# Optimization experiments

Hardware: AMD Instinct MI355X
Metric: run time of the kernel (lower is better)

The kernel has to match this reference:

```python
import jax, jax.numpy as jnp
import numpy as np

NUM_HEADS = 12
H = W = 64            # spatial grid (SAM ViT-B global attention)
DIM = 768
HEAD_DIM = DIM // NUM_HEADS


def setup_inputs() -> dict:
    key = jax.random.key(0)
    ks = jax.random.split(key, 7)
    return {
        "x": jax.random.normal(ks[0], (1, H, W, DIM), dtype=jnp.float32),
        "qkv_w": jax.random.normal(ks[1], (3 * DIM, DIM), dtype=jnp.float32) * 0.02,
        "qkv_b": jax.random.normal(ks[2], (3 * DIM,), dtype=jnp.float32) * 0.02,
        "proj_w": jax.random.normal(ks[3], (DIM, DIM), dtype=jnp.float32) * 0.02,
        "proj_b": jax.random.normal(ks[4], (DIM,), dtype=jnp.float32) * 0.02,
        "rel_pos_h": jax.random.normal(ks[5], (2 * H - 1, HEAD_DIM), dtype=jnp.float32) * 0.02,
        "rel_pos_w": jax.random.normal(ks[6], (2 * W - 1, HEAD_DIM), dtype=jnp.float32) * 0.02,
    }


def _get_rel_pos(size: int, rel_pos: jnp.ndarray) -> jnp.ndarray:
    # q_size == k_size == size; rel_pos already has length 2*size-1 (no interp).
    coords = jnp.arange(size)[:, None] - jnp.arange(size)[None, :] + (size - 1)
    return rel_pos[coords]  # [size, size, head_dim]


def reference(x, qkv_w, qkv_b, proj_w, proj_b, rel_pos_h, rel_pos_w):
    B, h, w, C = x.shape
    nh, hd = NUM_HEADS, C // NUM_HEADS
    S = h * w
    scale = hd ** -0.5

    qkv = x.reshape(B, S, C) @ qkv_w.T + qkv_b            # [B, S, 3C]
    qkv = qkv.reshape(B, S, 3, nh, hd).transpose(2, 0, 3, 1, 4)
    qkv = qkv.reshape(3, B * nh, S, hd)
    q, k, v = qkv[0], qkv[1], qkv[2]                      # [B*nh, S, hd]

    attn = jnp.einsum('bqc,bkc->bqk', q * scale, k)       # [B*nh, S, S]

    Rh = _get_rel_pos(h, rel_pos_h)                       # [h, h, hd]
    Rw = _get_rel_pos(w, rel_pos_w)                       # [w, w, hd]
    r_q = q.reshape(B * nh, h, w, hd)
    rel_h = jnp.einsum('bhwc,hkc->bhwk', r_q, Rh)         # [B*nh, h, w, h]
    rel_w = jnp.einsum('bhwc,wkc->bhwk', r_q, Rw)         # [B*nh, h, w, w]
    attn = (attn.reshape(B * nh, h, w, h, w)
            + rel_h[:, :, :, :, None]
            + rel_w[:, :, :, None, :]).reshape(B * nh, S, S)

    attn = jax.nn.softmax(attn, axis=-1)
    out = jnp.einsum('bqk,bkc->bqc', attn, v)             # [B*nh, S, hd]
    out = out.reshape(B, nh, h, w, hd).transpose(0, 2, 3, 1, 4).reshape(B, h, w, C)
    return out @ proj_w.T + proj_b
```

## Files before the change

### kernel.cpp

```cpp
#include <hip/hip_runtime.h>


typedef __bf16 bf16;
typedef __bf16 bf16x8 __attribute__((ext_vector_type(8)));
typedef __bf16 bf16x4 __attribute__((ext_vector_type(4)));
typedef float f32x4 __attribute__((ext_vector_type(4)));
typedef float f32x16 __attribute__((ext_vector_type(16)));
typedef unsigned int u32;

__device__ __forceinline__ f32x4 mfma16(bf16x8 a, bf16x8 b, f32x4 c) {
  return __builtin_amdgcn_mfma_f32_16x16x32_bf16(a, b, c, 0, 0, 0);
}
__device__ __forceinline__ f32x16 mfma32(bf16x8 a, bf16x8 b, f32x16 c) {
  return __builtin_amdgcn_mfma_f32_32x32x16_bf16(a, b, c, 0, 0, 0);
}

typedef const __attribute__((address_space(1))) void* gas_ptr;
typedef __attribute__((address_space(3))) void* las_ptr;
__device__ __forceinline__ void gl_lds16(const void* g, void* l) {
  __builtin_amdgcn_global_load_lds((gas_ptr)g, (las_ptr)l, 16, 0, 0);
}

#define L2E 1.4426950408889634f

__global__ __launch_bounds__(256) void cvt3(
    const float* __restrict__ a, bf16* __restrict__ oa,
    const float* __restrict__ b, bf16* __restrict__ ob,
    const float* __restrict__ c, bf16* __restrict__ oc) {
  int blk = blockIdx.x;
  const float* src;
  bf16* dst;
  int base;
  if (blk < 1536)       { src = a; dst = oa; base = blk; }
  else if (blk < 2400)  { src = b; dst = ob; base = blk - 1536; }
  else                  { src = c; dst = oc; base = blk - 2400; }
  int idx = (base * 256 + threadIdx.x) * 8;
  f32x4 x = *(const f32x4*)&src[idx];
  f32x4 y = *(const f32x4*)&src[idx + 4];
  bf16x8 o;
#pragma unroll
  for (int j = 0; j < 4; j++) { o[j] = (bf16)x[j]; o[j + 4] = (bf16)y[j]; }
  *(bf16x8*)&dst[idx] = o;
}

template <int MODE>
__global__ __launch_bounds__(256) void gemm128(
    const bf16* __restrict__ A, const bf16* __restrict__ B,
    const float* __restrict__ bias, int K, int N,
    bf16* __restrict__ q_s, bf16* __restrict__ k_s, bf16* __restrict__ v_t,
    float* __restrict__ outf) {
  __shared__ __align__(16) bf16 lbuf[2][128 * 32];
  bf16* lA = lbuf[0];
  bf16* lB = lbuf[1];
  const int tid = threadIdx.x;
  const int w = tid >> 6, l = tid & 63;
  const int n0 = blockIdx.x * 128, m0 = blockIdx.y * 128;

  f32x4 acc[4][4] = {};

  const int ch0 = w * 2, ch1 = ch0 + 1;
  const int r0 = ch0 * 16 + (l >> 2), r1 = ch1 * 16 + (l >> 2);
  const int ce = (l & 3) * 8;
  const int mw = (w & 1) * 64, nw = (w >> 1) * 64;

  for (int k0 = 0; k0 < K; k0 += 32) {
    __syncthreads();
    gl_lds16(&A[(size_t)(m0 + r0) * K + k0 + ce], &lA[ch0 * 512]);
    gl_lds16(&A[(size_t)(m0 + r1) * K + k0 + ce], &lA[ch1 * 512]);
    gl_lds16(&B[(size_t)(n0 + r0) * K + k0 + ce], &lB[ch0 * 512]);
    gl_lds16(&B[(size_t)(n0 + r1) * K + k0 + ce], &lB[ch1 * 512]);
    __syncthreads();
    bf16x8 af[4], bfr[4];
#pragma unroll
    for (int i = 0; i < 4; i++)
      af[i] = *(const bf16x8*)&lA[(mw + i * 16 + (l & 15)) * 32 + (l >> 4) * 8];
#pragma unroll
    for (int i = 0; i < 4; i++)
      bfr[i] = *(const bf16x8*)&lB[(nw + i * 16 + (l & 15)) * 32 + (l >> 4) * 8];
#pragma unroll
    for (int mi = 0; mi < 4; mi++)
#pragma unroll
      for (int ni = 0; ni < 4; ni++)
        acc[mi][ni] = mfma16(af[mi], bfr[ni], acc[mi][ni]);
  }

  if (MODE == 0 && n0 >= 1536) {
    bf16* Lt = &lbuf[0][0];
#pragma unroll 1
    for (int pass = 0; pass < 2; ++pass) {
      __syncthreads();
      if ((w >> 1) == pass) {
        char* R = (char*)Lt + (w & 1) * 8192;
#pragma unroll
        for (int ni = 0; ni < 4; ni++) {
          const float bv = bias[n0 + nw + ni * 16 + (l & 15)];
          const int nl = ni * 16 + (l & 15);
#pragma unroll
          for (int mi = 0; mi < 4; mi++)
#pragma unroll
            for (int i2 = 0; i2 < 2; i2++) {
              const int ml2 = (mi * 16 + (l >> 4) * 4 + i2 * 2) * 2;
              union { bf16 b[2]; u32 u; } pk;
              pk.b[0] = (bf16)(acc[mi][ni][i2 * 2] + bv);
              pk.b[1] = (bf16)(acc[mi][ni][i2 * 2 + 1] + bv);
              *(u32*)(R + nl * 128 + (ml2 ^ ((nl & 7) << 4))) = pk.u;
            }
        }
      }
      __syncthreads();
      if ((w >> 1) == pass) {
        const char* R = (const char*)Lt + (w & 1) * 8192;
#pragma unroll
        for (int r = 0; r < 8; r++) {
          const int nl = r * 8 + (l >> 3);
          const int pc = ((l & 7) * 16) ^ ((nl & 7) << 4);
          bf16x8 val = *(const bf16x8*)(R + nl * 128 + pc);
          const int n = n0 + pass * 64 + nl;
          const int head = (n - 1536) >> 6, hd = n & 63;
          *(bf16x8*)&v_t[((size_t)(head * 64 + hd)) * 4096 + m0 + (w & 1) * 64 +
                         (l & 7) * 8] = val;
        }
      }
    }
    return;
  }

#pragma unroll
  for (int ni = 0; ni < 4; ni++) {
    const int n = n0 + nw + ni * 16 + (l & 15);
    const float bv = bias[n];
#pragma unroll
    for (int mi = 0; mi < 4; mi++) {
#pragma unroll
      for (int i = 0; i < 4; i++) {
        const int m = m0 + mw + mi * 16 + (l >> 4) * 4 + i;
        const float v = acc[mi][ni][i] + bv;
        if (MODE == 0) {
          const int which = n / 768, hn = n % 768;
          const int head = hn >> 6, hd = hn & 63;
          if (which == 0)      q_s[((size_t)head * 4096 + m) * 64 + hd] = (bf16)v;
          else                 k_s[((size_t)head * 4096 + m) * 64 + hd] = (bf16)v;
        } else {
          outf[(size_t)m * N + n] = v;
        }
      }
    }
  }
}

__global__ __launch_bounds__(64) void rel_pos_w(
    const bf16* __restrict__ q_s, const float* __restrict__ table,
    float* __restrict__ out) {
  const int l = threadIdx.x;
  const int p = blockIdx.x, head = blockIdx.y;
  const size_t hbase = (size_t)head * 4096 * 64;

  f32x4 acc[4][4] = {};
#pragma unroll
  for (int ks = 0; ks < 2; ks++) {
    bf16x8 af[4], bfr[4];
#pragma unroll
    for (int mi = 0; mi < 4; mi++) {
      const int row = mi * 16 + (l & 15);
      const int s = row * 64 + p;
      af[mi] = *(const bf16x8*)&q_s[hbase + (size_t)s * 64 + ks * 32 + (l >> 4) * 8];
    }
#pragma unroll
    for (int ni = 0; ni < 4; ni++) {
      const int col = ni * 16 + (l & 15);
      const float* tp = &table[(size_t)(p - col + 63) * 64 + ks * 32 + (l >> 4) * 8];
      f32x4 t0 = *(const f32x4*)tp;
      f32x4 t1 = *(const f32x4*)(tp + 4);
      bf16x8 bb;
#pragma unroll
      for (int j = 0; j < 4; j++) { bb[j] = (bf16)t0[j]; bb[j + 4] = (bf16)t1[j]; }
      bfr[ni] = bb;
    }
#pragma unroll
    for (int mi = 0; mi < 4; mi++)
#pragma unroll
      for (int ni = 0; ni < 4; ni++)
        acc[mi][ni] = mfma16(af[mi], bfr[ni], acc[mi][ni]);
  }
#pragma unroll
  for (int mi = 0; mi < 4; mi++)
#pragma unroll
    for (int ni = 0; ni < 4; ni++)
#pragma unroll
      for (int i = 0; i < 4; i++) {
        const int row = mi * 16 + (l >> 4) * 4 + i;
        const int col = ni * 16 + (l & 15);
        const int sq = row * 64 + p;
        out[hbase + (size_t)sq * 64 + col] = acc[mi][ni][i];
      }
}

__global__ __launch_bounds__(256) void flash_attn(
    const bf16* __restrict__ q_s, const bf16* __restrict__ k_s,
    const bf16* __restrict__ v_t, const float* __restrict__ rph,
    const float* __restrict__ bias_w, bf16* __restrict__ attn_out) {
  __shared__ __align__(16) char smem[49408];
  float* lBH = (float*)(smem + 32768);

  const int tid = threadIdx.x;
  const int w = tid >> 6, l = tid & 63;
  const int r5 = l & 31, h = l >> 5, r7 = l & 7;
  const int qg = w & 1, kh2 = w >> 1;
  const int f = blockIdx.x;
  const int g = (f & 7) * 96 + (f >> 3);
  const int head = g >> 6, qh = g & 63;
  const size_t hbase = (size_t)head << 18;
  const int qloc = qg * 32 + r5;
  const size_t sq = (size_t)qh * 64 + qloc;

  const int ch0 = w * 2, ch1 = ch0 + 1;
  const int lr3 = l >> 3;
  const int swz = ((l & 7) ^ lr3) * 8;
  const bf16* kp0 = k_s + hbase + (size_t)(ch0 * 8 + lr3) * 64 + swz;
  const bf16* kp1 = k_s + hbase + (size_t)(ch1 * 8 + lr3) * 64 + swz;
  const bf16* vp0 = v_t + hbase + (size_t)(ch0 * 8 + lr3) * 4096 + swz;
  const bf16* vp1 = v_t + hbase + (size_t)(ch1 * 8 + lr3) * 4096 + swz;

#define STAGE(buf)                                                        \
  do {                                                                    \
    gl_lds16(kp0, smem + (buf) * 8192 + ch0 * 1024);                      \
    gl_lds16(kp1, smem + (buf) * 8192 + ch1 * 1024);                      \
    gl_lds16(vp0, smem + 16384 + (buf) * 8192 + ch0 * 1024);              \
    gl_lds16(vp1, smem + 16384 + (buf) * 8192 + ch1 * 1024);              \
  } while (0)

  STAGE(0);
  kp0 += 4096; kp1 += 4096; vp0 += 64; vp1 += 64;

  {
    const int q16 = l & 15, g4 = l >> 4;
    const size_t sq16 = (size_t)qh * 64 + w * 16 + q16;
    bf16x8 qf16[2];
    qf16[0] = *(const bf16x8*)&q_s[hbase + sq16 * 64 + g4 * 8];
    qf16[1] = *(const bf16x8*)&q_s[hbase + sq16 * 64 + 32 + g4 * 8];
    f32x4 abh[4] = {};
#pragma unroll
    for (int ks = 0; ks < 2; ks++)
#pragma unroll
      for (int ni = 0; ni < 4; ni++) {
        const int kh = ni * 16 + q16;
        const float* tp = &rph[(size_t)(qh + 63 - kh) * 64 + ks * 32 + g4 * 8];
        f32x4 t0 = *(const f32x4*)tp;
        f32x4 t1 = *(const f32x4*)(tp + 4);
        bf16x8 rf;
#pragma unroll
        for (int j = 0; j < 4; j++) { rf[j] = (bf16)t0[j]; rf[j + 4] = (bf16)t1[j]; }
        abh[ni] = mfma16(rf, qf16[ks], abh[ni]);
      }
#pragma unroll
    for (int ni = 0; ni < 4; ni++)
#pragma unroll
      for (int i = 0; i < 4; i++)
        lBH[(w * 16 + q16) * 65 + ni * 16 + g4 * 4 + i] = abh[ni][i];
  }

  bf16x8 qv[4];
#pragma unroll
  for (int s = 0; s < 4; s++)
    qv[s] = *(const bf16x8*)&q_s[hbase + sq * 64 + s * 16 + h * 8];

  float c2[16];
#pragma unroll
  for (int G = 0; G < 4; G++) {
    f32x4 cv = *(const f32x4*)&bias_w[hbase + sq * 64 + kh2 * 32 + G * 8 + h * 4];
#pragma unroll
    for (int i = 0; i < 4; i++) c2[G * 4 + i] = cv[i] * L2E;
  }

  int offK[4], offV[2][2];
  const int rowK = kh2 * 32 + r5;
#pragma unroll
  for (int s = 0; s < 4; s++)
    offK[s] = rowK * 128 + (((s * 2 + h) ^ r7) * 16);
#pragma unroll
  for (int T = 0; T < 2; T++)
#pragma unroll
    for (int st = 0; st < 2; st++)
      offV[T][st] = (T * 32 + r5) * 128 + (((kh2 * 4 + st * 2 + h) ^ r7) * 16);

  f32x16 o[2] = {};
  float mrun = -1e30f, lrun = 0.f;
  const float SC2 = 0.125f * L2E;

  auto compute = [&](int t) {
    const char* kb = smem + (t & 1) * 8192;
    const char* vb = smem + 16384 + (t & 1) * 8192;

    f32x16 sacc = {0.f, 0.f, 0.f, 0.f, 0.f, 0.f, 0.f, 0.f,
                   0.f, 0.f, 0.f, 0.f, 0.f, 0.f, 0.f, 0.f};
    __builtin_amdgcn_s_setprio(1);
#pragma unroll
    for (int s = 0; s < 4; s++) {
      bf16x8 kf = *(const bf16x8*)(kb + offK[s]);
      sacc = mfma32(kf, qv[s], sacc);
    }
    __builtin_amdgcn_s_setprio(0);

    float p[16], pm = -1e30f;
#pragma unroll
    for (int j = 0; j < 16; j++) {
      p[j] = sacc[j] * SC2 + c2[j];
      pm = fmaxf(pm, p[j]);
    }
    pm = fmaxf(pm, __shfl_xor(pm, 32, 64));
    const float bh2 = lBH[qloc * 65 + t] * L2E;
    const float rmf = pm + bh2;

    if (!__all(rmf - mrun <= 8.f)) {
      const float mn = fmaxf(mrun, rmf);
      const float al = __builtin_amdgcn_exp2f(mrun - mn);
      mrun = mn;
      lrun *= al;
      o[0] *= al;
      o[1] *= al;
    }

    const float d = bh2 - mrun;
    float rs = 0.f;
    u32 w8[8];
#pragma unroll
    for (int j = 0; j < 8; j++) {
      float e0 = __builtin_amdgcn_exp2f(p[2 * j] + d);
      float e1 = __builtin_amdgcn_exp2f(p[2 * j + 1] + d);
      rs += e0 + e1;
      union { bf16 b[2]; u32 u; } cvu;
      cvu.b[0] = (bf16)e0;
      cvu.b[1] = (bf16)e1;
      w8[j] = cvu.u;
    }
    rs += __shfl_xor(rs, 32, 64);
    lrun += rs;

#pragma unroll
    for (int st = 0; st < 2; st++) {
      u32 x0 = h ? w8[4 * st] : w8[4 * st + 2];
      u32 x1 = h ? w8[4 * st + 1] : w8[4 * st + 3];
      u32 p0 = (u32)__shfl_xor((int)x0, 32, 64);
      u32 p1 = (u32)__shfl_xor((int)x1, 32, 64);
      union { u32 u[4]; bf16x8 v; } pf;
      pf.u[0] = h ? p0 : w8[4 * st];
      pf.u[1] = h ? p1 : w8[4 * st + 1];
      pf.u[2] = h ? w8[4 * st + 2] : p0;
      pf.u[3] = h ? w8[4 * st + 3] : p1;
      __builtin_amdgcn_s_setprio(1);
#pragma unroll
      for (int T = 0; T < 2; T++) {
        bf16x8 vf = *(const bf16x8*)(vb + offV[T][st]);
        o[T] = mfma32(vf, pf.v, o[T]);
      }
      __builtin_amdgcn_s_setprio(0);
    }
  };

  __syncthreads();

  for (int t = 0; t < 63; t++) {
    STAGE((t + 1) & 1);
    kp0 += 4096; kp1 += 4096; vp0 += 64; vp1 += 64;
    asm volatile("s_waitcnt vmcnt(4)" ::: "memory");
    __builtin_amdgcn_s_barrier();
    __builtin_amdgcn_sched_barrier(0);
    compute(t);
    __builtin_amdgcn_s_barrier();
    __builtin_amdgcn_sched_barrier(0);
  }
  asm volatile("s_waitcnt vmcnt(0)" ::: "memory");
  __builtin_amdgcn_s_barrier();
  __builtin_amdgcn_sched_barrier(0);
  compute(63);
  __syncthreads();

  float* MM = (float*)smem;
  float* ML = (float*)(smem + 256);
  float* MO = (float*)(smem + 512);
  if (w >= 2) {
    if (h == 0) { MM[qg * 32 + r5] = mrun; ML[qg * 32 + r5] = lrun; }
#pragma unroll
    for (int T = 0; T < 2; T++)
#pragma unroll
      for (int G = 0; G < 4; G++) {
        f32x4 ov;
#pragma unroll
        for (int i = 0; i < 4; i++) ov[i] = o[T][4 * G + i];
        *(f32x4*)&MO[qg * 2048 + r5 * 64 + T * 32 + G * 8 + h * 4] = ov;
      }
  }
  __syncthreads();
  if (w < 2) {
    const float mp = MM[qg * 32 + r5], lp = ML[qg * 32 + r5];
    const float mT = fmaxf(mrun, mp);
    const float a = __builtin_amdgcn_exp2f(mrun - mT);
    const float b = __builtin_amdgcn_exp2f(mp - mT);
    const float inv = 1.f / (lrun * a + lp * b);
#pragma unroll
    for (int T = 0; T < 2; T++)
#pragma unroll
      for (int G = 0; G < 4; G++) {
        f32x4 po = *(const f32x4*)&MO[qg * 2048 + r5 * 64 + T * 32 + G * 8 + h * 4];
        bf16x4 ob;
#pragma unroll
        for (int i = 0; i < 4; i++)
          ob[i] = (bf16)((o[T][4 * G + i] * a + po[i] * b) * inv);
        *(bf16x4*)&attn_out[sq * 768 + head * 64 + T * 32 + G * 8 + h * 4] = ob;
      }
  }
#undef STAGE
}

extern "C" void kernel_launch(void* const* d_in, const int* in_sizes, int n_in,
                              void* d_out, int out_size, void* d_ws, size_t ws_size,
                              hipStream_t stream) {
  const float* x      = (const float*)d_in[0];
  const float* qkv_w  = (const float*)d_in[1];
  const float* qkv_b  = (const float*)d_in[2];
  const float* proj_w = (const float*)d_in[3];
  const float* proj_b = (const float*)d_in[4];
  const float* rph    = (const float*)d_in[5];
  const float* rpw    = (const float*)d_in[6];

  char* ws = (char*)d_ws;
  bf16*  xb    = (bf16*)(ws);
  bf16*  wqkv  = (bf16*)(ws + 6291456);
  bf16*  wproj = (bf16*)(ws + 9830400);
  bf16*  q_s   = (bf16*)(ws + 11010048);
  bf16*  k_s   = (bf16*)(ws + 17301504);
  bf16*  v_t   = (bf16*)(ws + 23592960);
  bf16*  attno = (bf16*)(ws + 29884416);
  float* bwv   = (float*)(ws + 36175872);

  cvt3<<<2688, 256, 0, stream>>>(x, xb, qkv_w, wqkv, proj_w, wproj);

  gemm128<0><<<dim3(18, 32), 256, 0, stream>>>(xb, wqkv, qkv_b, 768, 2304,
                                               q_s, k_s, v_t, nullptr);

  rel_pos_w<<<dim3(64, 12), 64, 0, stream>>>(q_s, rpw, bwv);

  flash_attn<<<768, 256, 0, stream>>>(q_s, k_s, v_t, rph, bwv, attno);

  gemm128<1><<<dim3(6, 32), 256, 0, stream>>>(attno, wproj, proj_b, 768, 768,
                                              nullptr, nullptr, nullptr,
                                              (float*)d_out);
}
```

Baseline: 253.5 us.

## Widen GEMM K-tile with swizzled LDS, use permlane32 swap in attention

The projection GEMM now stages 64-wide K tiles into XOR-swizzled LDS, which halves the number of barrier pairs per K loop and is meant to avoid bank conflicts on fragment reads. The flash attention K/V LDS swizzle is changed to also fold in the chunk index. Cross-half reductions and P-fragment exchanges use permlane32_swap where the builtin is available instead of ds_bpermute-based shuffles, which cuts LDS traffic and instruction count in the softmax inner loop. The trade-offs are doubled GEMM LDS use and reliance on the builtin being present, with a shuffle fallback otherwise.

```diff
diff --git a/kernel.cpp b/kernel.cpp
--- a/kernel.cpp
+++ b/kernel.cpp
@@ -19,6 +19,30 @@
 typedef __attribute__((address_space(3))) void* las_ptr;
 __device__ __forceinline__ void gl_lds16(const void* g, void* l) {
   __builtin_amdgcn_global_load_lds((gas_ptr)g, (las_ptr)l, 16, 0, 0);
+}
+
+#if defined(__has_builtin)
+#if __has_builtin(__builtin_amdgcn_permlane32_swap)
+#define HAVE_PLSWAP 1
+#endif
+#endif
+__device__ __forceinline__ void pswap_u(u32& a, u32& b) {
+#ifdef HAVE_PLSWAP
+  auto r = __builtin_amdgcn_permlane32_swap(a, b, false, false);
+  a = r[0]; b = r[1];
+#else
+  const bool hi = (threadIdx.x & 32) != 0;
+  u32 sa = (u32)__shfl_xor((int)a, 32, 64);
+  u32 sb = (u32)__shfl_xor((int)b, 32, 64);
+  u32 na = hi ? sb : a;
+  u32 nb = hi ? b : sa;
+  a = na; b = nb;
+#endif
+}
+__device__ __forceinline__ void pswap_f(float& a, float& b) {
+  u32 x = __float_as_uint(a), y = __float_as_uint(b);
+  pswap_u(x, y);
+  a = __uint_as_float(x); b = __uint_as_float(y);
 }
 
 #define L2E 1.4426950408889634f
@@ -49,43 +73,56 @@
     const float* __restrict__ bias, int K, int N,
     bf16* __restrict__ q_s, bf16* __restrict__ k_s, bf16* __restrict__ v_t,
     float* __restrict__ outf) {
-  __shared__ __align__(16) bf16 lbuf[2][128 * 32];
-  bf16* lA = lbuf[0];
-  bf16* lB = lbuf[1];
+  __shared__ __align__(16) bf16 lA[128 * 64];
+  __shared__ __align__(16) bf16 lB[128 * 64];
   const int tid = threadIdx.x;
   const int w = tid >> 6, l = tid & 63;
   const int n0 = blockIdx.x * 128, m0 = blockIdx.y * 128;
 
   f32x4 acc[4][4] = {};
 
-  const int ch0 = w * 2, ch1 = ch0 + 1;
-  const int r0 = ch0 * 16 + (l >> 2), r1 = ch1 * 16 + (l >> 2);
-  const int ce = (l & 3) * 8;
+  int rowc[4], sloc[4];
+#pragma unroll
+  for (int j = 0; j < 4; j++) {
+    const int c = w * 4 + j;
+    rowc[j] = c * 8 + (l >> 3);
+    sloc[j] = (((l & 7) ^ (l >> 3) ^ c) & 7) * 8;
+  }
   const int mw = (w & 1) * 64, nw = (w >> 1) * 64;
 
-  for (int k0 = 0; k0 < K; k0 += 32) {
+  for (int k0 = 0; k0 < K; k0 += 64) {
     __syncthreads();
-    gl_lds16(&A[(size_t)(m0 + r0) * K + k0 + ce], &lA[ch0 * 512]);
-    gl_lds16(&A[(size_t)(m0 + r1) * K + k0 + ce], &lA[ch1 * 512]);
-    gl_lds16(&B[(size_t)(n0 + r0) * K + k0 + ce], &lB[ch0 * 512]);
-    gl_lds16(&B[(size_t)(n0 + r1) * K + k0 + ce], &lB[ch1 * 512]);
+#pragma unroll
+    for (int j = 0; j < 4; j++) {
+      gl_lds16(&A[(size_t)(m0 + rowc[j]) * K + k0 + sloc[j]],
+               (char*)lA + (w * 4 + j) * 1024);
+      gl_lds16(&B[(size_t)(n0 + rowc[j]) * K + k0 + sloc[j]],
+               (char*)lB + (w * 4 + j) * 1024);
+    }
     __syncthreads();
-    bf16x8 af[4], bfr[4];
-#pragma unroll
-    for (int i = 0; i < 4; i++)
-      af[i] = *(const bf16x8*)&lA[(mw + i * 16 + (l & 15)) * 32 + (l >> 4) * 8];
-#pragma unroll
-    for (int i = 0; i < 4; i++)
-      bfr[i] = *(const bf16x8*)&lB[(nw + i * 16 + (l & 15)) * 32 + (l >> 4) * 8];
-#pragma unroll
-    for (int mi = 0; mi < 4; mi++)
-#pragma unroll
-      for (int ni = 0; ni < 4; ni++)
-        acc[mi][ni] = mfma16(af[mi], bfr[ni], acc[mi][ni]);
+    bf16x8 af[2][4], bfr[2][4];
+#pragma unroll
+    for (int ks = 0; ks < 2; ks++)
+#pragma unroll
+      for (int i = 0; i < 4; i++) {
+        const int rA = mw + i * 16 + (l & 15);
+        const int rB = nw + i * 16 + (l & 15);
+        const int slot = ks * 4 + (l >> 4);
+        const int fA = ((rA ^ (rA >> 3)) & 7), fB = ((rB ^ (rB >> 3)) & 7);
+        af[ks][i] = *(const bf16x8*)((const char*)lA + rA * 128 + ((slot ^ fA) & 7) * 16);
+        bfr[ks][i] = *(const bf16x8*)((const char*)lB + rB * 128 + ((slot ^ fB) & 7) * 16);
+      }
+#pragma unroll
+    for (int ks = 0; ks < 2; ks++)
+#pragma unroll
+      for (int mi = 0; mi < 4; mi++)
+#pragma unroll
+        for (int ni = 0; ni < 4; ni++)
+          acc[mi][ni] = mfma16(af[ks][mi], bfr[ks][ni], acc[mi][ni]);
   }
 
   if (MODE == 0 && n0 >= 1536) {
-    bf16* Lt = &lbuf[0][0];
+    bf16* Lt = lA;
 #pragma unroll 1
     for (int pass = 0; pass < 2; ++pass) {
       __syncthreads();
@@ -204,7 +241,7 @@
 
   const int tid = threadIdx.x;
   const int w = tid >> 6, l = tid & 63;
-  const int r5 = l & 31, h = l >> 5, r7 = l & 7;
+  const int r5 = l & 31, h = l >> 5;
   const int qg = w & 1, kh2 = w >> 1;
   const int f = blockIdx.x;
   const int g = (f & 7) * 96 + (f >> 3);
@@ -215,11 +252,12 @@
 
   const int ch0 = w * 2, ch1 = ch0 + 1;
   const int lr3 = l >> 3;
-  const int swz = ((l & 7) ^ lr3) * 8;
-  const bf16* kp0 = k_s + hbase + (size_t)(ch0 * 8 + lr3) * 64 + swz;
-  const bf16* kp1 = k_s + hbase + (size_t)(ch1 * 8 + lr3) * 64 + swz;
-  const bf16* vp0 = v_t + hbase + (size_t)(ch0 * 8 + lr3) * 4096 + swz;
-  const bf16* vp1 = v_t + hbase + (size_t)(ch1 * 8 + lr3) * 4096 + swz;
+  const int swz0 = (((l & 7) ^ lr3 ^ ch0) & 7) * 8;
+  const int swz1 = (((l & 7) ^ lr3 ^ ch1) & 7) * 8;
+  const bf16* kp0 = k_s + hbase + (size_t)(ch0 * 8 + lr3) * 64 + swz0;
+  const bf16* kp1 = k_s + hbase + (size_t)(ch1 * 8 + lr3) * 64 + swz1;
+  const bf16* vp0 = v_t + hbase + (size_t)(ch0 * 8 + lr3) * 4096 + swz0;
+  const bf16* vp1 = v_t + hbase + (size_t)(ch1 * 8 + lr3) * 4096 + swz1;
 
 #define STAGE(buf)                                                        \
   do {                                                                    \
@@ -274,14 +312,17 @@
 
   int offK[4], offV[2][2];
   const int rowK = kh2 * 32 + r5;
+  const int fK = ((l & 7) ^ (kh2 * 4 + ((l >> 3) & 3))) & 7;
 #pragma unroll
   for (int s = 0; s < 4; s++)
-    offK[s] = rowK * 128 + (((s * 2 + h) ^ r7) * 16);
-#pragma unroll
-  for (int T = 0; T < 2; T++)
+    offK[s] = rowK * 128 + (((s * 2 + h) ^ fK) & 7) * 16;
+#pragma unroll
+  for (int T = 0; T < 2; T++) {
+    const int fV = ((l & 7) ^ (T * 4 + ((l >> 3) & 3))) & 7;
 #pragma unroll
     for (int st = 0; st < 2; st++)
-      offV[T][st] = (T * 32 + r5) * 128 + (((kh2 * 4 + st * 2 + h) ^ r7) * 16);
+      offV[T][st] = (T * 32 + r5) * 128 + (((kh2 * 4 + st * 2 + h) ^ fV) & 7) * 16;
+  }
 
   f32x16 o[2] = {};
   float mrun = -1e30f, lrun = 0.f;
@@ -307,7 +348,7 @@
       p[j] = sacc[j] * SC2 + c2[j];
       pm = fmaxf(pm, p[j]);
     }
-    pm = fmaxf(pm, __shfl_xor(pm, 32, 64));
+    { float t2 = pm; pswap_f(t2, pm); pm = fmaxf(t2, pm); }
     const float bh2 = lBH[qloc * 65 + t] * L2E;
     const float rmf = pm + bh2;
 
@@ -333,20 +374,17 @@
       cvu.b[1] = (bf16)e1;
       w8[j] = cvu.u;
     }
-    rs += __shfl_xor(rs, 32, 64);
+    { float t2 = rs; pswap_f(t2, rs); rs = t2 + rs; }
     lrun += rs;
 
 #pragma unroll
     for (int st = 0; st < 2; st++) {
-      u32 x0 = h ? w8[4 * st] : w8[4 * st + 2];
-      u32 x1 = h ? w8[4 * st + 1] : w8[4 * st + 3];
-      u32 p0 = (u32)__shfl_xor((int)x0, 32, 64);
-      u32 p1 = (u32)__shfl_xor((int)x1, 32, 64);
       union { u32 u[4]; bf16x8 v; } pf;
-      pf.u[0] = h ? p0 : w8[4 * st];
-      pf.u[1] = h ? p1 : w8[4 * st + 1];
-      pf.u[2] = h ? w8[4 * st + 2] : p0;
-      pf.u[3] = h ? w8[4 * st + 3] : p1;
+      u32 a0 = w8[4 * st], b0 = w8[4 * st + 2];
+      u32 a1 = w8[4 * st + 1], b1 = w8[4 * st + 3];
+      pswap_u(a0, b0);
+      pswap_u(a1, b1);
+      pf.u[0] = a0; pf.u[1] = a1; pf.u[2] = b0; pf.u[3] = b1;
       __builtin_amdgcn_s_setprio(1);
 #pragma unroll
       for (int T = 0; T < 2; T++) {
```

After: 241.7 us. 1.05x faster.
